# Performance work log

Measured on AMD Instinct MI355X. Metric: run time of the kernel, lower is better.

Reference implementation:

```python
import jax, jax.numpy as jnp
import numpy as np

C = 1024
H = 16

def setup_inputs() -> dict:
    key = jax.random.key(0)
    ks = jax.random.split(key, 12)
    s = lambda d: 1.0 / np.sqrt(d)
    return {
        "x": jax.random.normal(ks[0], (2, 2048, C), dtype=jnp.float32),
        "ln1_g": jnp.ones((C,), jnp.float32),
        "ln1_b": jnp.zeros((C,), jnp.float32),
        "attn_w": jax.random.normal(ks[1], (C, 3 * C), jnp.float32) * s(C),
        "attn_b": jnp.zeros((3 * C,), jnp.float32),
        "proj_w": jax.random.normal(ks[2], (C, C), jnp.float32) * s(C),
        "proj_b": jnp.zeros((C,), jnp.float32),
        "ln2_g": jnp.ones((C,), jnp.float32),
        "ln2_b": jnp.zeros((C,), jnp.float32),
        "fc_w": jax.random.normal(ks[3], (C, 4 * C), jnp.float32) * s(C),
        "fc_b": jnp.zeros((4 * C,), jnp.float32),
        "fc2_w": jax.random.normal(ks[4], (4 * C, C), jnp.float32) * s(4 * C),
        "fc2_b": jnp.zeros((C,), jnp.float32),
    }

def _layernorm(x, g, b, eps=1e-5):
    mu = jnp.mean(x, axis=-1, keepdims=True)
    var = jnp.var(x, axis=-1, keepdims=True)
    return (x - mu) * jax.lax.rsqrt(var + eps) * g + b

def _attn(x, attn_w, attn_b, proj_w, proj_b):
    B, T, Cd = x.shape
    hd = Cd // H
    qkv = x @ attn_w + attn_b                      # [B,T,3C]
    q, k, v = jnp.split(qkv, 3, axis=-1)
    q = q.reshape(B, T, H, hd).transpose(0, 2, 1, 3)  # [B,H,T,hd]
    k = k.reshape(B, T, H, hd).transpose(0, 2, 1, 3)
    v = v.reshape(B, T, H, hd).transpose(0, 2, 1, 3)
    att = jnp.einsum("bhqd,bhkd->bhqk", q, k) * (1.0 / np.sqrt(hd))
    mask = jnp.tril(jnp.ones((T, T), bool))
    att = jnp.where(mask, att, -jnp.inf)
    att = jax.nn.softmax(att, axis=-1)
    y = jnp.einsum("bhqk,bhkd->bhqd", att, v)
    y = y.transpose(0, 2, 1, 3).reshape(B, T, Cd)
    return y @ proj_w + proj_b

def _mlp(x, fc_w, fc_b, fc2_w, fc2_b):
    h = jax.nn.gelu(x @ fc_w + fc_b, approximate=False)
    return h @ fc2_w + fc2_b

def reference(x, ln1_g, ln1_b, attn_w, attn_b, proj_w, proj_b,
              ln2_g, ln2_b, fc_w, fc_b, fc2_w, fc2_b):
    x = x + _attn(_layernorm(x, ln1_g, ln1_b), attn_w, attn_b, proj_w, proj_b)
    x = x + _mlp(_layernorm(x, ln2_g, ln2_b), fc_w, fc_b, fc2_w, fc2_b)
    return x
```

## Files before the change

### kernel.cpp

```cpp
#include <hip/hip_runtime.h>
#include <hip/hip_bf16.h>
#include <math.h>

typedef __attribute__((ext_vector_type(8))) short short8;
typedef __attribute__((ext_vector_type(4))) float f32x4;

#define C_DIM 1024
#define T_DIM 2048
#define NH 16
#define HD 64
#define NTOK 4096

__device__ __forceinline__ unsigned short f2bf(float f) {
  unsigned u = __float_as_uint(f);
  u += 0x7fffu + ((u >> 16) & 1u);
  return (unsigned short)(u >> 16);
}

__global__ __launch_bounds__(256) void ln_kernel(
    const float* __restrict__ x, const float* __restrict__ g,
    const float* __restrict__ b, unsigned short* __restrict__ out) {
  int row = blockIdx.x;
  int tid = threadIdx.x;
  const float4* xr = (const float4*)(x + (size_t)row * C_DIM);
  float4 v = xr[tid];
  float s = v.x + v.y + v.z + v.w;
  float ss = v.x * v.x + v.y * v.y + v.z * v.z + v.w * v.w;
#pragma unroll
  for (int off = 32; off; off >>= 1) {
    s += __shfl_down(s, off);
    ss += __shfl_down(ss, off);
  }
  __shared__ float red[8];
  if ((tid & 63) == 0) { red[tid >> 6] = s; red[4 + (tid >> 6)] = ss; }
  __syncthreads();
  float S = red[0] + red[1] + red[2] + red[3];
  float SS = red[4] + red[5] + red[6] + red[7];
  float mu = S * (1.0f / C_DIM);
  float var = SS * (1.0f / C_DIM) - mu * mu;
  float rs = rsqrtf(var + 1e-5f);
  float4 gg = ((const float4*)g)[tid];
  float4 bb = ((const float4*)b)[tid];
  ushort4 o;
  o.x = f2bf((v.x - mu) * rs * gg.x + bb.x);
  o.y = f2bf((v.y - mu) * rs * gg.y + bb.y);
  o.z = f2bf((v.z - mu) * rs * gg.z + bb.z);
  o.w = f2bf((v.w - mu) * rs * gg.w + bb.w);
  *(ushort4*)(out + (size_t)row * C_DIM + tid * 4) = o;
}

__global__ __launch_bounds__(256) void wt_kernel(
    const float* __restrict__ W, unsigned short* __restrict__ Wt, int K, int N) {
  __shared__ float t[32][33];
  int n0 = blockIdx.x * 32, k0 = blockIdx.y * 32;
  int tx = threadIdx.x, ty = threadIdx.y;
#pragma unroll
  for (int j = 0; j < 4; j++)
    t[ty + j * 8][tx] = W[(size_t)(k0 + ty + j * 8) * N + n0 + tx];
  __syncthreads();
#pragma unroll
  for (int j = 0; j < 4; j++)
    Wt[(size_t)(n0 + ty + j * 8) * K + k0 + tx] = f2bf(t[tx][ty + j * 8]);
}

template <int ACT, int OUTBF>
__global__ __launch_bounds__(256) void gemm_bt(
    const unsigned short* __restrict__ A, const unsigned short* __restrict__ Bt,
    const float* __restrict__ bias, const float* __restrict__ res,
    void* __restrict__ Cout, int M, int N, int K) {
  __shared__ short sA[128 * 32];
  __shared__ short sB[128 * 32];
  int tid = threadIdx.x;
  int wave = tid >> 6, lane = tid & 63;
  int l16 = lane & 15, quad = lane >> 4;
  int row0 = blockIdx.y * 128, col0 = blockIdx.x * 128;
  int wm = (wave & 1) * 64, wn = (wave >> 1) * 64;
  f32x4 acc[4][4];
#pragma unroll
  for (int i = 0; i < 4; i++)
#pragma unroll
    for (int j = 0; j < 4; j++) acc[i][j] = (f32x4){0.f, 0.f, 0.f, 0.f};

  int r1 = tid >> 2, cc1 = (tid & 3) * 8;
  const unsigned short* Ap = A + (size_t)(row0 + r1) * K + cc1;
  const unsigned short* Bp = Bt + (size_t)(col0 + r1) * K + cc1;
  const size_t RSK = (size_t)64 * K;
  uint4 pa0 = *(const uint4*)Ap;
  uint4 pa1 = *(const uint4*)(Ap + RSK);
  uint4 pb0 = *(const uint4*)Bp;
  uint4 pb1 = *(const uint4*)(Bp + RSK);

  for (int k0 = 0; k0 < K; k0 += 32) {
    if (k0) __syncthreads();
    *(uint4*)&sA[r1 * 32 + cc1] = pa0;
    *(uint4*)&sA[(r1 + 64) * 32 + cc1] = pa1;
    *(uint4*)&sB[r1 * 32 + cc1] = pb0;
    *(uint4*)&sB[(r1 + 64) * 32 + cc1] = pb1;
    __syncthreads();
    if (k0 + 32 < K) {
      pa0 = *(const uint4*)(Ap + k0 + 32);
      pa1 = *(const uint4*)(Ap + RSK + k0 + 32);
      pb0 = *(const uint4*)(Bp + k0 + 32);
      pb1 = *(const uint4*)(Bp + RSK + k0 + 32);
    }
    short8 a[4], b[4];
#pragma unroll
    for (int i = 0; i < 4; i++) {
      a[i] = *(const short8*)&sA[(wm + i * 16 + l16) * 32 + quad * 8];
      b[i] = *(const short8*)&sB[(wn + i * 16 + l16) * 32 + quad * 8];
    }
#pragma unroll
    for (int mi = 0; mi < 4; mi++)
#pragma unroll
      for (int ni = 0; ni < 4; ni++)
        acc[mi][ni] = __builtin_amdgcn_mfma_f32_16x16x32_bf16(a[mi], b[ni], acc[mi][ni], 0, 0, 0);
  }
#pragma unroll
  for (int mi = 0; mi < 4; mi++) {
#pragma unroll
    for (int ni = 0; ni < 4; ni++) {
      int col = col0 + wn + ni * 16 + l16;
      float bv = bias[col];
#pragma unroll
      for (int i = 0; i < 4; i++) {
        int row = row0 + wm + mi * 16 + quad * 4 + i;
        float v = acc[mi][ni][i] + bv;
        if (ACT == 1) v = 0.5f * v * (1.0f + erff(v * 0.7071067811865475f));
        if (res) v += res[(size_t)row * N + col];
        if (OUTBF)
          ((unsigned short*)Cout)[(size_t)row * N + col] = f2bf(v);
        else
          ((float*)Cout)[(size_t)row * N + col] = v;
      }
    }
  }
}

#define AP 72
__global__ __launch_bounds__(256) void attn_mfma_kernel(
    const unsigned short* __restrict__ qkv, unsigned short* __restrict__ Y) {
  __shared__ short sK[64 * AP];
  __shared__ short sVt[64 * AP];
  __shared__ short sP[4][16 * AP];
  int qt = gridDim.x - 1 - blockIdx.x;
  int hb = blockIdx.y;
  int bb = hb >> 4, h = hb & 15;
  int tid = threadIdx.x, wave = tid >> 6, lane = tid & 63;
  int l16 = lane & 15, quad = lane >> 4;
  int qbase = qt * 64 + wave * 16;

  const unsigned short* qrow = qkv + (size_t)(bb * T_DIM + qbase + l16) * 3072 + h * HD;
  short8 qf[2];
  qf[0] = *(const short8*)(qrow + quad * 8);
  qf[1] = *(const short8*)(qrow + 32 + quad * 8);

  f32x4 o[4];
#pragma unroll
  for (int i = 0; i < 4; i++) o[i] = (f32x4){0.f, 0.f, 0.f, 0.f};
  float m = -1e30f, l = 0.f;

  const unsigned short* Kbase = qkv + (size_t)bb * T_DIM * 3072 + C_DIM + h * HD;
  const unsigned short* Vbase = Kbase + C_DIM;

  int rr = tid >> 3, dcg = tid & 7, dc = dcg * 8;
  const unsigned short* Kp = Kbase + (size_t)rr * 3072 + dc;
  const unsigned short* Vp = Vbase + (size_t)rr * 3072 + dc;
  const size_t HROW = (size_t)32 * 3072;
  const size_t TS = (size_t)64 * 3072;

  uint4 kx0 = *(const uint4*)Kp;
  uint4 kx1 = *(const uint4*)(Kp + HROW);
  uint4 vx0 = *(const uint4*)Vp;
  uint4 vx1 = *(const uint4*)(Vp + HROW);

  for (int kt = 0; kt <= qt; kt++) {
    int kv0 = kt * 64;
    if (kt) __syncthreads();
    *(uint4*)&sK[rr * AP + dc] = kx0;
    *(uint4*)&sK[(rr + 32) * AP + dc] = kx1;
    {
      unsigned short ve[8];
      *(uint4*)ve = vx0;
#pragma unroll
      for (int j = 0; j < 8; j++) {
        int jj = (j + rr + dcg) & 7;
        sVt[(dc + jj) * AP + rr] = (short)ve[jj];
      }
      *(uint4*)ve = vx1;
#pragma unroll
      for (int j = 0; j < 8; j++) {
        int jj = (j + rr + 32 + dcg) & 7;
        sVt[(dc + jj) * AP + rr + 32] = (short)ve[jj];
      }
    }
    __syncthreads();
    if (kt < qt) {
      const unsigned short* Kn = Kp + (size_t)(kt + 1) * TS;
      const unsigned short* Vn = Vp + (size_t)(kt + 1) * TS;
      kx0 = *(const uint4*)Kn;
      kx1 = *(const uint4*)(Kn + HROW);
      vx0 = *(const uint4*)Vn;
      vx1 = *(const uint4*)(Vn + HROW);
    }

    f32x4 st[4];
#pragma unroll
    for (int i = 0; i < 4; i++) st[i] = (f32x4){0.f, 0.f, 0.f, 0.f};
#pragma unroll
    for (int kc = 0; kc < 2; kc++)
#pragma unroll
      for (int mt = 0; mt < 4; mt++) {
        short8 af = *(const short8*)&sK[(mt * 16 + l16) * AP + kc * 32 + quad * 8];
        st[mt] = __builtin_amdgcn_mfma_f32_16x16x32_bf16(af, qf[kc], st[mt], 0, 0, 0);
      }

    float vals[16];
    if (kt == qt) {
      int qg = qbase + l16;
#pragma unroll
      for (int mt = 0; mt < 4; mt++)
#pragma unroll
        for (int r = 0; r < 4; r++) {
          int kv = kv0 + mt * 16 + quad * 4 + r;
          vals[mt * 4 + r] = (kv <= qg) ? st[mt][r] * 0.125f : -1e30f;
        }
    } else {
#pragma unroll
      for (int mt = 0; mt < 4; mt++)
#pragma unroll
        for (int r = 0; r < 4; r++) vals[mt * 4 + r] = st[mt][r] * 0.125f;
    }
    float mx = vals[0];
#pragma unroll
    for (int i = 1; i < 16; i++) mx = fmaxf(mx, vals[i]);
    mx = fmaxf(mx, __shfl_xor(mx, 16));
    mx = fmaxf(mx, __shfl_xor(mx, 32));
    float mnew = fmaxf(m, mx);
    float alpha = __expf(m - mnew);
    float ps = 0.f;
#pragma unroll
    for (int i = 0; i < 16; i++) {
      vals[i] = __expf(vals[i] - mnew);
      ps += vals[i];
    }
    ps += __shfl_xor(ps, 16);
    ps += __shfl_xor(ps, 32);
    l = l * alpha + ps;
    m = mnew;
#pragma unroll
    for (int r = 0; r < 4; r++) {
      float ar = __shfl(alpha, quad * 20 + r);
#pragma unroll
      for (int dt = 0; dt < 4; dt++) o[dt][r] *= ar;
    }

#pragma unroll
    for (int mt = 0; mt < 4; mt++) {
      ushort4 pw;
      pw.x = f2bf(vals[mt * 4 + 0]);
      pw.y = f2bf(vals[mt * 4 + 1]);
      pw.z = f2bf(vals[mt * 4 + 2]);
      pw.w = f2bf(vals[mt * 4 + 3]);
      *(ushort4*)&sP[wave][l16 * AP + mt * 16 + quad * 4] = pw;
    }

#pragma unroll
    for (int kc = 0; kc < 2; kc++) {
      short8 pa = *(const short8*)&sP[wave][l16 * AP + kc * 32 + quad * 8];
#pragma unroll
      for (int dt = 0; dt < 4; dt++) {
        short8 vb = *(const short8*)&sVt[(dt * 16 + l16) * AP + kc * 32 + quad * 8];
        o[dt] = __builtin_amdgcn_mfma_f32_16x16x32_bf16(pa, vb, o[dt], 0, 0, 0);
      }
    }
  }

  float il[4];
#pragma unroll
  for (int r = 0; r < 4; r++) il[r] = 1.0f / __shfl(l, quad * 20 + r);
  unsigned short* Yb = Y + (size_t)(bb * T_DIM + qbase) * C_DIM + h * HD;
#pragma unroll
  for (int dt = 0; dt < 4; dt++)
#pragma unroll
    for (int r = 0; r < 4; r++)
      Yb[(size_t)(quad * 4 + r) * C_DIM + dt * 16 + l16] = f2bf(o[dt][r] * il[r]);
}

extern "C" void kernel_launch(void* const* d_in, const int* in_sizes, int n_in,
                              void* d_out, int out_size, void* d_ws, size_t ws_size,
                              hipStream_t stream) {
  const float* x      = (const float*)d_in[0];
  const float* ln1_g  = (const float*)d_in[1];
  const float* ln1_b  = (const float*)d_in[2];
  const float* attn_w = (const float*)d_in[3];
  const float* attn_b = (const float*)d_in[4];
  const float* proj_w = (const float*)d_in[5];
  const float* proj_b = (const float*)d_in[6];
  const float* ln2_g  = (const float*)d_in[7];
  const float* ln2_b  = (const float*)d_in[8];
  const float* fc_w   = (const float*)d_in[9];
  const float* fc_b   = (const float*)d_in[10];
  const float* fc2_w  = (const float*)d_in[11];
  const float* fc2_b  = (const float*)d_in[12];

  char* ws = (char*)d_ws;
  unsigned short* wqkv_t  = (unsigned short*)(ws + 0);
  unsigned short* wproj_t = (unsigned short*)(ws + 6291456);
  unsigned short* wfc_t   = (unsigned short*)(ws + 8388608);
  unsigned short* wfc2_t  = (unsigned short*)(ws + 16777216);
  unsigned short* xn1     = (unsigned short*)(ws + 25165824);
  unsigned short* qkv     = (unsigned short*)(ws + 33554432);
  unsigned short* y       = (unsigned short*)(ws + 58720256);
  unsigned short* hmid    = (unsigned short*)(ws + 33554432);
  unsigned short* xn2     = xn1;
  float* x1  = (float*)d_out;
  float* out = (float*)d_out;

  dim3 t32x8(32, 8);
  wt_kernel<<<dim3(3072 / 32, 1024 / 32), t32x8, 0, stream>>>(attn_w, wqkv_t, 1024, 3072);
  wt_kernel<<<dim3(1024 / 32, 1024 / 32), t32x8, 0, stream>>>(proj_w, wproj_t, 1024, 1024);
  wt_kernel<<<dim3(4096 / 32, 1024 / 32), t32x8, 0, stream>>>(fc_w, wfc_t, 1024, 4096);
  wt_kernel<<<dim3(1024 / 32, 4096 / 32), t32x8, 0, stream>>>(fc2_w, wfc2_t, 4096, 1024);

  ln_kernel<<<NTOK, 256, 0, stream>>>(x, ln1_g, ln1_b, xn1);
  gemm_bt<0, 1><<<dim3(3072 / 128, NTOK / 128), 256, 0, stream>>>(
      xn1, wqkv_t, attn_b, nullptr, qkv, NTOK, 3072, 1024);
  attn_mfma_kernel<<<dim3(T_DIM / 64, 32), 256, 0, stream>>>(qkv, y);
  gemm_bt<0, 0><<<dim3(1024 / 128, NTOK / 128), 256, 0, stream>>>(
      y, wproj_t, proj_b, x, (void*)x1, NTOK, 1024, 1024);
  ln_kernel<<<NTOK, 256, 0, stream>>>(x1, ln2_g, ln2_b, xn2);
  gemm_bt<1, 1><<<dim3(4096 / 128, NTOK / 128), 256, 0, stream>>>(
      xn2, wfc_t, fc_b, nullptr, hmid, NTOK, 4096, 1024);
  gemm_bt<0, 0><<<dim3(1024 / 128, NTOK / 128), 256, 0, stream>>>(
      hmid, wfc2_t, fc2_b, x1, (void*)out, NTOK, 1024, 4096);
}
```

Before: 472.3 us.

## Pre-transpose V globally and stream K/V from registers in attention

```diff
diff --git a/kernel.cpp b/kernel.cpp
--- a/kernel.cpp
+++ b/kernel.cpp
@@ -63,6 +63,22 @@
     Wt[(size_t)(n0 + ty + j * 8) * K + k0 + tx] = f2bf(t[tx][ty + j * 8]);
 }
 
+__global__ __launch_bounds__(256) void vt_kernel(
+    const unsigned short* __restrict__ qkv, unsigned short* __restrict__ Vt) {
+  __shared__ unsigned short t[32][34];
+  int hb = blockIdx.z, bb = hb >> 4, h = hb & 15;
+  int t0 = blockIdx.x * 32, d0 = blockIdx.y * 32;
+  int tx = threadIdx.x, ty = threadIdx.y;
+#pragma unroll
+  for (int j = 0; j < 4; j++)
+    t[ty + j * 8][tx] =
+        qkv[(size_t)(bb * T_DIM + t0 + ty + j * 8) * 3072 + 2048 + h * HD + d0 + tx];
+  __syncthreads();
+#pragma unroll
+  for (int j = 0; j < 4; j++)
+    Vt[((size_t)hb * HD + d0 + ty + j * 8) * T_DIM + t0 + tx] = t[tx][ty + j * 8];
+}
+
 template <int ACT, int OUTBF>
 __global__ __launch_bounds__(256) void gemm_bt(
     const unsigned short* __restrict__ A, const unsigned short* __restrict__ Bt,
@@ -136,89 +152,71 @@
   }
 }
 
-#define AP 72
-__global__ __launch_bounds__(256) void attn_mfma_kernel(
-    const unsigned short* __restrict__ qkv, unsigned short* __restrict__ Y) {
-  __shared__ short sK[64 * AP];
-  __shared__ short sVt[64 * AP];
-  __shared__ short sP[4][16 * AP];
-  int qt = gridDim.x - 1 - blockIdx.x;
-  int hb = blockIdx.y;
-  int bb = hb >> 4, h = hb & 15;
+__global__ __launch_bounds__(128) void attn_mfma_kernel(
+    const unsigned short* __restrict__ qkv, const unsigned short* __restrict__ Vt,
+    unsigned short* __restrict__ Y) {
+  __shared__ short sP[2][16 * 36];
+  int hb = blockIdx.y, bb = hb >> 4, h = hb & 15;
   int tid = threadIdx.x, wave = tid >> 6, lane = tid & 63;
   int l16 = lane & 15, quad = lane >> 4;
-  int qbase = qt * 64 + wave * 16;
+  int qidx = wave ? (127 - (int)blockIdx.x) : (int)blockIdx.x;
+  int qbase = qidx * 16;
+  int ntiles = (qidx >> 1) + 1;
 
   const unsigned short* qrow = qkv + (size_t)(bb * T_DIM + qbase + l16) * 3072 + h * HD;
   short8 qf[2];
   qf[0] = *(const short8*)(qrow + quad * 8);
   qf[1] = *(const short8*)(qrow + 32 + quad * 8);
 
+  const unsigned short* Kb = qkv + (size_t)bb * T_DIM * 3072 + C_DIM + h * HD;
+  const unsigned short* Vb = Vt + (size_t)hb * HD * T_DIM;
+
   f32x4 o[4];
 #pragma unroll
   for (int i = 0; i < 4; i++) o[i] = (f32x4){0.f, 0.f, 0.f, 0.f};
   float m = -1e30f, l = 0.f;
 
-  const unsigned short* Kbase = qkv + (size_t)bb * T_DIM * 3072 + C_DIM + h * HD;
-  const unsigned short* Vbase = Kbase + C_DIM;
-
-  int rr = tid >> 3, dcg = tid & 7, dc = dcg * 8;
-  const unsigned short* Kp = Kbase + (size_t)rr * 3072 + dc;
-  const unsigned short* Vp = Vbase + (size_t)rr * 3072 + dc;
-  const size_t HROW = (size_t)32 * 3072;
-  const size_t TS = (size_t)64 * 3072;
-
-  uint4 kx0 = *(const uint4*)Kp;
-  uint4 kx1 = *(const uint4*)(Kp + HROW);
-  uint4 vx0 = *(const uint4*)Vp;
-  uint4 vx1 = *(const uint4*)(Vp + HROW);
-
-  for (int kt = 0; kt <= qt; kt++) {
-    int kv0 = kt * 64;
-    if (kt) __syncthreads();
-    *(uint4*)&sK[rr * AP + dc] = kx0;
-    *(uint4*)&sK[(rr + 32) * AP + dc] = kx1;
-    {
-      unsigned short ve[8];
-      *(uint4*)ve = vx0;
-#pragma unroll
-      for (int j = 0; j < 8; j++) {
-        int jj = (j + rr + dcg) & 7;
-        sVt[(dc + jj) * AP + rr] = (short)ve[jj];
-      }
-      *(uint4*)ve = vx1;
-#pragma unroll
-      for (int j = 0; j < 8; j++) {
-        int jj = (j + rr + 32 + dcg) & 7;
-        sVt[(dc + jj) * AP + rr + 32] = (short)ve[jj];
-      }
-    }
-    __syncthreads();
-    if (kt < qt) {
-      const unsigned short* Kn = Kp + (size_t)(kt + 1) * TS;
-      const unsigned short* Vn = Vp + (size_t)(kt + 1) * TS;
-      kx0 = *(const uint4*)Kn;
-      kx1 = *(const uint4*)(Kn + HROW);
-      vx0 = *(const uint4*)Vn;
-      vx1 = *(const uint4*)(Vn + HROW);
-    }
-
-    f32x4 st[4];
-#pragma unroll
-    for (int i = 0; i < 4; i++) st[i] = (f32x4){0.f, 0.f, 0.f, 0.f};
+  short8 ck[4], cv[4];
+#pragma unroll
+  for (int mt = 0; mt < 2; mt++)
 #pragma unroll
     for (int kc = 0; kc < 2; kc++)
-#pragma unroll
-      for (int mt = 0; mt < 4; mt++) {
-        short8 af = *(const short8*)&sK[(mt * 16 + l16) * AP + kc * 32 + quad * 8];
-        st[mt] = __builtin_amdgcn_mfma_f32_16x16x32_bf16(af, qf[kc], st[mt], 0, 0, 0);
-      }
-
-    float vals[16];
-    if (kt == qt) {
+      ck[mt * 2 + kc] =
+          *(const short8*)(Kb + (size_t)(mt * 16 + l16) * 3072 + kc * 32 + quad * 8);
+#pragma unroll
+  for (int dt = 0; dt < 4; dt++)
+    cv[dt] = *(const short8*)(Vb + (size_t)(dt * 16 + l16) * T_DIM + quad * 8);
+
+  for (int kt = 0; kt < ntiles; kt++) {
+    int kv0 = kt * 32;
+    short8 nk[4], nv[4];
+    if (kt + 1 < ntiles) {
+      int nv0 = kv0 + 32;
+#pragma unroll
+      for (int mt = 0; mt < 2; mt++)
+#pragma unroll
+        for (int kc = 0; kc < 2; kc++)
+          nk[mt * 2 + kc] = *(const short8*)(Kb + (size_t)(nv0 + mt * 16 + l16) * 3072 +
+                                             kc * 32 + quad * 8);
+#pragma unroll
+      for (int dt = 0; dt < 4; dt++)
+        nv[dt] = *(const short8*)(Vb + (size_t)(dt * 16 + l16) * T_DIM + nv0 + quad * 8);
+    }
+
+    f32x4 st[2];
+    st[0] = (f32x4){0.f, 0.f, 0.f, 0.f};
+    st[1] = (f32x4){0.f, 0.f, 0.f, 0.f};
+#pragma unroll
+    for (int kc = 0; kc < 2; kc++)
+#pragma unroll
+      for (int mt = 0; mt < 2; mt++)
+        st[mt] = __builtin_amdgcn_mfma_f32_16x16x32_bf16(ck[mt * 2 + kc], qf[kc], st[mt], 0, 0, 0);
+
+    float vals[8];
+    if (kt == ntiles - 1) {
       int qg = qbase + l16;
 #pragma unroll
-      for (int mt = 0; mt < 4; mt++)
+      for (int mt = 0; mt < 2; mt++)
 #pragma unroll
         for (int r = 0; r < 4; r++) {
           int kv = kv0 + mt * 16 + quad * 4 + r;
@@ -226,20 +224,20 @@
         }
     } else {
 #pragma unroll
-      for (int mt = 0; mt < 4; mt++)
+      for (int mt = 0; mt < 2; mt++)
 #pragma unroll
         for (int r = 0; r < 4; r++) vals[mt * 4 + r] = st[mt][r] * 0.125f;
     }
     float mx = vals[0];
 #pragma unroll
-    for (int i = 1; i < 16; i++) mx = fmaxf(mx, vals[i]);
+    for (int i = 1; i < 8; i++) mx = fmaxf(mx, vals[i]);
     mx = fmaxf(mx, __shfl_xor(mx, 16));
     mx = fmaxf(mx, __shfl_xor(mx, 32));
     float mnew = fmaxf(m, mx);
     float alpha = __expf(m - mnew);
     float ps = 0.f;
 #pragma unroll
-    for (int i = 0; i < 16; i++) {
+    for (int i = 0; i < 8; i++) {
       vals[i] = __expf(vals[i] - mnew);
       ps += vals[i];
     }
@@ -255,23 +253,22 @@
     }
 
 #pragma unroll
-    for (int mt = 0; mt < 4; mt++) {
+    for (int mt = 0; mt < 2; mt++) {
       ushort4 pw;
       pw.x = f2bf(vals[mt * 4 + 0]);
       pw.y = f2bf(vals[mt * 4 + 1]);
       pw.z = f2bf(vals[mt * 4 + 2]);
       pw.w = f2bf(vals[mt * 4 + 3]);
-      *(ushort4*)&sP[wave][l16 * AP + mt * 16 + quad * 4] = pw;
-    }
-
-#pragma unroll
-    for (int kc = 0; kc < 2; kc++) {
-      short8 pa = *(const short8*)&sP[wave][l16 * AP + kc * 32 + quad * 8];
-#pragma unroll
-      for (int dt = 0; dt < 4; dt++) {
-        short8 vb = *(const short8*)&sVt[(dt * 16 + l16) * AP + kc * 32 + quad * 8];
-        o[dt] = __builtin_amdgcn_mfma_f32_16x16x32_bf16(pa, vb, o[dt], 0, 0, 0);
-      }
+      *(ushort4*)&sP[wave][l16 * 36 + mt * 16 + quad * 4] = pw;
+    }
+    short8 pa = *(const short8*)&sP[wave][l16 * 36 + quad * 8];
+#pragma unroll
+    for (int dt = 0; dt < 4; dt++)
+      o[dt] = __builtin_amdgcn_mfma_f32_16x16x32_bf16(pa, cv[dt], o[dt], 0, 0, 0);
+#pragma unroll
+    for (int i = 0; i < 4; i++) {
+      ck[i] = nk[i];
+      cv[i] = nv[i];
     }
   }
 
@@ -311,6 +308,7 @@
   unsigned short* xn1     = (unsigned short*)(ws + 25165824);
   unsigned short* qkv     = (unsigned short*)(ws + 33554432);
   unsigned short* y       = (unsigned short*)(ws + 58720256);
+  unsigned short* Vtb     = (unsigned short*)(ws + 67108864);
   unsigned short* hmid    = (unsigned short*)(ws + 33554432);
   unsigned short* xn2     = xn1;
   float* x1  = (float*)d_out;
@@ -325,7 +323,8 @@
   ln_kernel<<<NTOK, 256, 0, stream>>>(x, ln1_g, ln1_b, xn1);
   gemm_bt<0, 1><<<dim3(3072 / 128, NTOK / 128), 256, 0, stream>>>(
       xn1, wqkv_t, attn_b, nullptr, qkv, NTOK, 3072, 1024);
-  attn_mfma_kernel<<<dim3(T_DIM / 64, 32), 256, 0, stream>>>(qkv, y);
+  vt_kernel<<<dim3(T_DIM / 32, HD / 32, 32), t32x8, 0, stream>>>(qkv, Vtb);
+  attn_mfma_kernel<<<dim3(128 / 2, 32), 128, 0, stream>>>(qkv, Vtb, y);
   gemm_bt<0, 0><<<dim3(1024 / 128, NTOK / 128), 256, 0, stream>>>(
       y, wproj_t, proj_b, x, (void*)x1, NTOK, 1024, 1024);
   ln_kernel<<<NTOK, 256, 0, stream>>>(x1, ln2_g, ln2_b, xn2);
```

Measured after the change: 503.7 us. 1.07x slower.
